# Optimization experiments

Hardware: AMD Instinct MI355X
Metric: run time of the kernel (lower is better)

The kernel has to match this reference:

```python
import jax, jax.numpy as jnp
import numpy as np

HID = 256
BN_EPS = 1e-5
LN_EPS = 1e-5


def setup_inputs() -> dict:
    key = jax.random.key(0)
    ks = jax.random.split(key, 32)
    N, E, B = 50000, 400000, 2048
    F_ATOM, F_PROT = 70, 480

    def lin(k, fi, fo):
        return jax.random.normal(k, (fi, fo), jnp.float32) / np.sqrt(fi).astype(np.float32)

    inp = {
        "x": jax.random.normal(ks[0], (N, F_ATOM), jnp.float32),
        "edge_index": jax.random.randint(ks[1], (2, E), 0, N, jnp.int64),
        "batch": jnp.sort(jax.random.randint(ks[2], (N,), 0, B, jnp.int64)),
        "protein_emb": jax.random.normal(ks[3], (B, F_PROT), jnp.float32),
        # GIN layer 0 (70 -> 256)
        "gin0_w1": lin(ks[4], F_ATOM, HID), "gin0_b1": jnp.zeros((HID,), jnp.float32),
        "gin0_w2": lin(ks[5], HID, HID),    "gin0_b2": jnp.zeros((HID,), jnp.float32),
        "gin0_gamma": jnp.ones((HID,), jnp.float32), "gin0_beta": jnp.zeros((HID,), jnp.float32),
        # GIN layers 1..3 stacked (256 -> 256)
        "gin_w1": jnp.stack([lin(ks[6 + i], HID, HID) for i in range(3)]),
        "gin_b1": jnp.zeros((3, HID), jnp.float32),
        "gin_w2": jnp.stack([lin(ks[9 + i], HID, HID) for i in range(3)]),
        "gin_b2": jnp.zeros((3, HID), jnp.float32),
        "gin_gamma": jnp.ones((3, HID), jnp.float32),
        "gin_beta": jnp.zeros((3, HID), jnp.float32),
        # protein projector
        "wp": lin(ks[12], F_PROT, HID), "bp": jnp.zeros((HID,), jnp.float32),
        "ln_g": jnp.ones((HID,), jnp.float32), "ln_b": jnp.zeros((HID,), jnp.float32),
        # predictor MLP
        "wpr1": lin(ks[13], 2 * HID, 1024), "bpr1": jnp.zeros((1024,), jnp.float32),
        "wpr2": lin(ks[14], 1024, 512),     "bpr2": jnp.zeros((512,), jnp.float32),
        "wpr3": lin(ks[15], 512, 1),        "bpr3": jnp.zeros((1,), jnp.float32),
    }
    return inp


def _gin_layer(h, src, dst, n_nodes, w1, b1, w2, b2, gamma, beta):
    # GINConv (eps=0): mlp(x + sum_{j->i} x_j); scatter-add over destination
    agg = jax.ops.segment_sum(h[src], dst, num_segments=n_nodes)
    z = h + agg
    z = jax.nn.relu(z @ w1 + b1) @ w2 + b2
    # BatchNorm1d in eval mode: running_mean=0, running_var=1
    z = z * (gamma / np.sqrt(1.0 + BN_EPS).astype(np.float32)) + beta
    return jax.nn.relu(z)  # dropout is identity in eval


def reference(x, edge_index, batch, protein_emb,
              gin0_w1, gin0_b1, gin0_w2, gin0_b2, gin0_gamma, gin0_beta,
              gin_w1, gin_b1, gin_w2, gin_b2, gin_gamma, gin_beta,
              wp, bp, ln_g, ln_b,
              wpr1, bpr1, wpr2, bpr2, wpr3, bpr3):
    n_nodes = x.shape[0]
    n_graphs = protein_emb.shape[0]
    src, dst = edge_index[0], edge_index[1]

    h = _gin_layer(x, src, dst, n_nodes, gin0_w1, gin0_b1, gin0_w2, gin0_b2, gin0_gamma, gin0_beta)
    for i in range(3):  # layers 1..3 with residual
        h = h + _gin_layer(h, src, dst, n_nodes,
                           gin_w1[i], gin_b1[i], gin_w2[i], gin_b2[i], gin_gamma[i], gin_beta[i])

    # global_add_pool over graph ids
    drug_vec = jax.ops.segment_sum(h, batch, num_segments=n_graphs)  # [B, 256]

    # protein projector: Linear -> LayerNorm -> ReLU (dropout identity)
    p = protein_emb @ wp + bp
    mu = jnp.mean(p, axis=-1, keepdims=True)
    var = jnp.var(p, axis=-1, keepdims=True)
    p = (p - mu) * jax.lax.rsqrt(var + LN_EPS) * ln_g + ln_b
    prot_vec = jax.nn.relu(p)

    cat = jnp.concatenate([drug_vec, prot_vec], axis=1)  # [B, 512]
    h1 = jax.nn.relu(cat @ wpr1 + bpr1)
    h2 = jax.nn.relu(h1 @ wpr2 + bpr2)
    return h2 @ wpr3 + bpr3  # [B, 1]
```

## Files before the change

kernel.cpp:

```cpp
#include <hip/hip_runtime.h>

#define F_ATOM 70

#define FLAG_RELU 1
#define FLAG_BN   2
#define FLAG_RES  4

typedef __attribute__((ext_vector_type(8))) short short8;
typedef __attribute__((ext_vector_type(4))) float floatx4;

__device__ __forceinline__ float bf2f(unsigned short u) {
    union { unsigned int i; float f; } x; x.i = (unsigned int)u << 16; return x.f;
}
__device__ __forceinline__ unsigned short f2bf(float f) {
    union { float f; unsigned int i; } x; x.f = f;
    unsigned int r = x.i + 0x7fffu + ((x.i >> 16) & 1u);
    return (unsigned short)(r >> 16);
}
__device__ __forceinline__ float blo(unsigned int u){ union{unsigned int a; float f;}x; x.a=u<<16; return x.f; }
__device__ __forceinline__ float bhi(unsigned int u){ union{unsigned int a; float f;}x; x.a=u&0xffff0000u; return x.f; }


__global__ void count_kernel(const int* __restrict__ dst, int* __restrict__ cnt, int E) {
    int i = blockIdx.x * blockDim.x + threadIdx.x;
    if (i < E) atomicAdd(&cnt[dst[i]], 1);
}

__global__ void scan_kernel(const int* __restrict__ cnt, int* __restrict__ offs, int n) {
    __shared__ int wsum[16];
    __shared__ int carry_s;
    int t = threadIdx.x, lane = t & 63, wid = t >> 6;
    if (t == 0) carry_s = 0;
    __syncthreads();
    for (int base = 0; base < n; base += 1024) {
        int idx = base + t;
        int v = (idx < n) ? cnt[idx] : 0;
        int s = v;
        #pragma unroll
        for (int o = 1; o < 64; o <<= 1) {
            int x = __shfl_up(s, o);
            if (lane >= o) s += x;
        }
        if (lane == 63) wsum[wid] = s;
        __syncthreads();
        int woff = 0;
        #pragma unroll
        for (int wI = 0; wI < 16; ++wI) woff += (wI < wid) ? wsum[wI] : 0;
        int carry = carry_s;
        if (idx < n) offs[idx] = carry + woff + s - v;
        __syncthreads();
        if (t == 1023) carry_s = carry + woff + s;
        __syncthreads();
    }
    if (threadIdx.x == 0) offs[n] = carry_s;
}

__global__ void fill_kernel(const int* __restrict__ src, const int* __restrict__ dst,
                            const int* __restrict__ offs, int* __restrict__ cursor,
                            int* __restrict__ ssrc, int E) {
    int i = blockIdx.x * blockDim.x + threadIdx.x;
    if (i < E) {
        int d = dst[i];
        int pos = atomicAdd(&cursor[d], 1);
        ssrc[offs[d] + pos] = src[i];
    }
}

__global__ void graph_bounds_kernel(const int* __restrict__ batch, int* __restrict__ goffs,
                                    int N, int B) {
    int g = blockIdx.x * blockDim.x + threadIdx.x;
    if (g > B) return;
    int lo = 0, hi = N;
    while (lo < hi) {
        int mid = (lo + hi) >> 1;
        if (batch[mid] < g) lo = mid + 1; else hi = mid;
    }
    goffs[g] = lo;
}


__global__ void wtrans_kernel(const float* __restrict__ src, unsigned short* __restrict__ dst,
                              int K, int NC, int Kpad, int L) {
    int idx = blockIdx.x * blockDim.x + threadIdx.x;
    int per = NC * Kpad;
    if (idx >= per * L) return;
    int l = idx / per; int r2 = idx - l * per;
    int nrow = r2 / Kpad, k = r2 - nrow * Kpad;
    float v = (k < K) ? src[(size_t)l * K * NC + (size_t)k * NC + nrow] : 0.f;
    dst[idx] = f2bf(v);
}

__global__ void cvt_kernel(const float* __restrict__ src, unsigned short* __restrict__ dst, int n) {
    int i = blockIdx.x * blockDim.x + threadIdx.x;
    if (i < n) dst[i] = f2bf(src[i]);
}

__global__ void agg0_kernel(const float* __restrict__ x, const int* __restrict__ offs,
                            const int* __restrict__ ssrc, unsigned short* __restrict__ z0, int n) {
    long long idx = (long long)blockIdx.x * blockDim.x + threadIdx.x;
    if (idx >= (long long)n * 128) return;
    int node = (int)(idx >> 7);
    int f = (int)(idx & 127);
    float a = 0.f;
    if (f < F_ATOM) {
        a = x[(long long)node * F_ATOM + f];
        int s = offs[node], e = offs[node + 1];
        for (int i = s; i < e; ++i) a += x[(long long)ssrc[i] * F_ATOM + f];
    }
    z0[idx] = f2bf(a);
}

__global__ void agg_bf16_kernel(const unsigned short* __restrict__ h, const int* __restrict__ offs,
                                const int* __restrict__ ssrc, unsigned short* __restrict__ out, int n) {
    int t = threadIdx.x;
    int node = blockIdx.x * 8 + (t >> 5);
    if (node >= n) return;
    int f8 = (t & 31) * 8;
    uint4 v = *(const uint4*)(h + (size_t)node * 256 + f8);
    float acc[8];
    acc[0]=blo(v.x); acc[1]=bhi(v.x); acc[2]=blo(v.y); acc[3]=bhi(v.y);
    acc[4]=blo(v.z); acc[5]=bhi(v.z); acc[6]=blo(v.w); acc[7]=bhi(v.w);
    int s = offs[node], e = offs[node + 1];
    for (int i = s; i < e; ++i) {
        uint4 u = *(const uint4*)(h + (size_t)ssrc[i] * 256 + f8);
        acc[0]+=blo(u.x); acc[1]+=bhi(u.x); acc[2]+=blo(u.y); acc[3]+=bhi(u.y);
        acc[4]+=blo(u.z); acc[5]+=bhi(u.z); acc[6]+=blo(u.w); acc[7]+=bhi(u.w);
    }
    unsigned int o0 = (unsigned int)f2bf(acc[0]) | ((unsigned int)f2bf(acc[1]) << 16);
    unsigned int o1 = (unsigned int)f2bf(acc[2]) | ((unsigned int)f2bf(acc[3]) << 16);
    unsigned int o2 = (unsigned int)f2bf(acc[4]) | ((unsigned int)f2bf(acc[5]) << 16);
    unsigned int o3 = (unsigned int)f2bf(acc[6]) | ((unsigned int)f2bf(acc[7]) << 16);
    *(uint4*)(out + (size_t)node * 256 + f8) = make_uint4(o0, o1, o2, o3);
}


template<int KSH>
__global__ __launch_bounds__(512) void fused_gin(
    const unsigned short* __restrict__ Z, const unsigned short* __restrict__ W1,
    const float* __restrict__ b1, const unsigned short* __restrict__ W2,
    const float* __restrict__ b2, const float* __restrict__ bng,
    const float* __restrict__ bnb, const unsigned short* __restrict__ res,
    unsigned short* __restrict__ out, int M)
{
    constexpr int CPR = KSH / 8;
    constexpr int NT1 = KSH / 32;
    __shared__ unsigned short sZ[128 * 256];
    const int T = threadIdx.x;
    const int lane = T & 63;
    const int w = T >> 6, wr = w >> 2, wc = w & 3;
    const int fr = lane & 15, hi = lane >> 4;
    const int crow = hi * 4;
    const int row0 = blockIdx.x * 128;

    #pragma unroll
    for (int i = 0; i < (128 * CPR) / 512; ++i) {
        int c = T + i * 512;
        int row = c / CPR, p = c % CPR;
        int pp = p ^ (row & 15);
        int gr = row0 + row; if (gr > M - 1) gr = M - 1;
        __builtin_amdgcn_global_load_lds(
            (const __attribute__((address_space(1))) void*)(Z + (size_t)gr * KSH + pp * 8),
            (__attribute__((address_space(3))) void*)&sZ[c * 8], 16, 0, 0);
    }
    __syncthreads();

    floatx4 acc[4][4];
    #pragma unroll
    for (int m = 0; m < 4; ++m)
        #pragma unroll
        for (int n = 0; n < 4; ++n)
            acc[m][n] = (floatx4){0.f, 0.f, 0.f, 0.f};

    {
        short8 cur[4], nxt[4];
        #pragma unroll
        for (int n = 0; n < 4; ++n)
            cur[n] = *(const short8*)(W1 + (size_t)(wc * 64 + n * 16 + fr) * KSH + hi * 8);
        #pragma unroll
        for (int kk = 0; kk < NT1; ++kk) {
            if (kk + 1 < NT1) {
                #pragma unroll
                for (int n = 0; n < 4; ++n)
                    nxt[n] = *(const short8*)(W1 + (size_t)(wc * 64 + n * 16 + fr) * KSH + (kk + 1) * 32 + hi * 8);
            }
            short8 af[4];
            #pragma unroll
            for (int m = 0; m < 4; ++m) {
                int r = wr * 64 + m * 16 + fr;
                int byte = r * (KSH * 2) + ((kk * 64 + hi * 16) ^ ((r & 15) << 4));
                af[m] = *(const short8*)((const char*)sZ + byte);
            }
            #pragma unroll
            for (int m = 0; m < 4; ++m)
                #pragma unroll
                for (int n = 0; n < 4; ++n)
                    acc[m][n] = __builtin_amdgcn_mfma_f32_16x16x32_bf16(af[m], cur[n], acc[m][n], 0, 0, 0);
            #pragma unroll
            for (int n = 0; n < 4; ++n) cur[n] = nxt[n];
        }
    }
    __syncthreads();

    #pragma unroll
    for (int n = 0; n < 4; ++n) {
        int col = wc * 64 + n * 16 + fr;
        float bb = b1[col];
        #pragma unroll
        for (int m = 0; m < 4; ++m) {
            #pragma unroll
            for (int j = 0; j < 4; ++j) {
                int r = wr * 64 + m * 16 + crow + j;
                float y = fmaxf(acc[m][n][j] + bb, 0.f);
                int byte = r * 512 + ((col * 2) ^ ((r & 15) << 4));
                *(unsigned short*)((char*)sZ + byte) = f2bf(y);
            }
        }
    }
    __syncthreads();

    #pragma unroll
    for (int m = 0; m < 4; ++m)
        #pragma unroll
        for (int n = 0; n < 4; ++n)
            acc[m][n] = (floatx4){0.f, 0.f, 0.f, 0.f};
    {
        short8 cur[4], nxt[4];
        #pragma unroll
        for (int n = 0; n < 4; ++n)
            cur[n] = *(const short8*)(W2 + (size_t)(wc * 64 + n * 16 + fr) * 256 + hi * 8);
        #pragma unroll
        for (int kk = 0; kk < 8; ++kk) {
            if (kk < 7) {
                #pragma unroll
                for (int n = 0; n < 4; ++n)
                    nxt[n] = *(const short8*)(W2 + (size_t)(wc * 64 + n * 16 + fr) * 256 + (kk + 1) * 32 + hi * 8);
            }
            short8 af[4];
            #pragma unroll
            for (int m = 0; m < 4; ++m) {
                int r = wr * 64 + m * 16 + fr;
                int byte = r * 512 + ((kk * 64 + hi * 16) ^ ((r & 15) << 4));
                af[m] = *(const short8*)((const char*)sZ + byte);
            }
            #pragma unroll
            for (int m = 0; m < 4; ++m)
                #pragma unroll
                for (int n = 0; n < 4; ++n)
                    acc[m][n] = __builtin_amdgcn_mfma_f32_16x16x32_bf16(af[m], cur[n], acc[m][n], 0, 0, 0);
            #pragma unroll
            for (int n = 0; n < 4; ++n) cur[n] = nxt[n];
        }
    }
    __syncthreads();

    {
        const float inv = rsqrtf(1.f + 1e-5f);
        #pragma unroll
        for (int n = 0; n < 4; ++n) {
            int col = wc * 64 + n * 16 + fr;
            float bb = b2[col];
            float sc = bng[col] * inv, be = bnb[col];
            #pragma unroll
            for (int m = 0; m < 4; ++m) {
                #pragma unroll
                for (int j = 0; j < 4; ++j) {
                    int r = wr * 64 + m * 16 + crow + j;
                    float y = (acc[m][n][j] + bb) * sc + be;
                    y = fmaxf(y, 0.f);
                    int byte = r * 512 + ((col * 2) ^ ((r & 15) << 4));
                    *(unsigned short*)((char*)sZ + byte) = f2bf(y);
                }
            }
        }
    }
    __syncthreads();

    #pragma unroll
    for (int i = 0; i < 8; ++i) {
        int c = T + i * 512;
        int row = c >> 5, slot = c & 31;
        int gr = row0 + row;
        if (gr >= M) continue;
        int byte = row * 512 + ((slot * 16) ^ ((row & 15) << 4));
        short8 v = *(const short8*)((const char*)sZ + byte);
        if (res) {
            short8 rv = *(const short8*)(res + (size_t)gr * 256 + slot * 8);
            #pragma unroll
            for (int e = 0; e < 8; ++e) {
                float f = bf2f((unsigned short)v[e]) + bf2f((unsigned short)rv[e]);
                v[e] = (short)f2bf(f);
            }
        }
        *(short8*)(out + (size_t)gr * 256 + slot * 8) = v;
    }
}


__global__ __launch_bounds__(256) void mfma_gemm(
    const unsigned short* __restrict__ A, const unsigned short* __restrict__ Bt,
    const float* __restrict__ bias, const float* __restrict__ bng,
    const float* __restrict__ bnb, const unsigned short* __restrict__ res,
    unsigned short* __restrict__ out, int M, int K, int NC, int flags)
{
    __shared__ unsigned short sA[2][128 * 32];
    __shared__ unsigned short sB[2][128 * 32];
    const int T = threadIdx.x;
    const int lane = T & 63;
    const int w = T >> 6, wr = w >> 1, wc = w & 1;
    const int row0 = blockIdx.x * 128;
    const int col0 = blockIdx.y * 128;
    const int nt = K >> 5;

    floatx4 acc[4][4];
    #pragma unroll
    for (int m = 0; m < 4; ++m)
        #pragma unroll
        for (int n = 0; n < 4; ++n)
            acc[m][n] = (floatx4){0.f, 0.f, 0.f, 0.f};

    auto stage = [&](int buf, int k0) {
        #pragma unroll
        for (int it = 0; it < 2; ++it) {
            int c = T + it * 256;
            int r = c >> 2, p = c & 3;
            int gr = row0 + r; if (gr > M - 1) gr = M - 1;
            const unsigned short* gA = A + (size_t)gr * K + k0 + p * 8;
            __builtin_amdgcn_global_load_lds(
                (const __attribute__((address_space(1))) void*)gA,
                (__attribute__((address_space(3))) void*)&sA[buf][c * 8], 16, 0, 0);
            const unsigned short* gB = Bt + (size_t)(col0 + r) * K + k0 + p * 8;
            __builtin_amdgcn_global_load_lds(
                (const __attribute__((address_space(1))) void*)gB,
                (__attribute__((address_space(3))) void*)&sB[buf][c * 8], 16, 0, 0);
        }
    };

    auto compute = [&](int buf) {
        const int fr = lane & 15;
        const int kh = (lane >> 4) * 8;
        short8 af[4], bv[4];
        #pragma unroll
        for (int m = 0; m < 4; ++m)
            af[m] = *(const short8*)&sA[buf][(wr * 64 + m * 16 + fr) * 32 + kh];
        #pragma unroll
        for (int n = 0; n < 4; ++n)
            bv[n] = *(const short8*)&sB[buf][(wc * 64 + n * 16 + fr) * 32 + kh];
        #pragma unroll
        for (int m = 0; m < 4; ++m)
            #pragma unroll
            for (int n = 0; n < 4; ++n)
                acc[m][n] = __builtin_amdgcn_mfma_f32_16x16x32_bf16(af[m], bv[n], acc[m][n], 0, 0, 0);
    };

    stage(0, 0);
    __syncthreads();
    int cur = 0;
    for (int t = 0; t < nt - 1; ++t) {
        stage(cur ^ 1, (t + 1) * 32);
        compute(cur);
        __syncthreads();
        cur ^= 1;
    }
    compute(cur);

    const int crow = (lane >> 4) * 4;
    const int ccol = lane & 15;
    const float inv = rsqrtf(1.f + 1e-5f);
    #pragma unroll
    for (int n = 0; n < 4; ++n) {
        int col = col0 + wc * 64 + n * 16 + ccol;
        float bb = bias ? bias[col] : 0.f;
        float sc = 1.f, be = 0.f;
        if (flags & FLAG_BN) { sc = bng[col] * inv; be = bnb[col]; }
        #pragma unroll
        for (int m = 0; m < 4; ++m) {
            #pragma unroll
            for (int j = 0; j < 4; ++j) {
                int r = row0 + wr * 64 + m * 16 + crow + j;
                if (r >= M) continue;
                float y = acc[m][n][j] + bb;
                if (flags & FLAG_BN) y = y * sc + be;
                if (flags & FLAG_RELU) y = fmaxf(y, 0.f);
                if (flags & FLAG_RES) y += bf2f(res[(size_t)r * NC + col]);
                out[(size_t)r * NC + col] = f2bf(y);
            }
        }
    }
}


__global__ void pool_kernel(const unsigned short* __restrict__ h, const int* __restrict__ goffs,
                            unsigned short* __restrict__ out, int ldout) {
    int g = blockIdx.x;
    int f = threadIdx.x;
    int s = goffs[g], e = goffs[g + 1];
    float acc = 0.f;
    for (int i = s; i < e; ++i) acc += bf2f(h[(size_t)i * 256 + f]);
    out[(size_t)g * ldout + f] = f2bf(acc);
}

__global__ void ln_relu_kernel(const unsigned short* __restrict__ p, const float* __restrict__ g,
                               const float* __restrict__ b, unsigned short* __restrict__ out, int ldout) {
    int row = blockIdx.x;
    int t = threadIdx.x;
    float v = bf2f(p[(size_t)row * 256 + t]);
    float s1 = v, s2 = v * v;
    #pragma unroll
    for (int o = 32; o > 0; o >>= 1) { s1 += __shfl_xor(s1, o); s2 += __shfl_xor(s2, o); }
    __shared__ float as1[4], as2[4];
    int w = t >> 6, lane = t & 63;
    if (lane == 0) { as1[w] = s1; as2[w] = s2; }
    __syncthreads();
    float tot1 = as1[0] + as1[1] + as1[2] + as1[3];
    float tot2 = as2[0] + as2[1] + as2[2] + as2[3];
    float mean = tot1 * (1.f / 256.f);
    float var = tot2 * (1.f / 256.f) - mean * mean;
    float y = (v - mean) * rsqrtf(var + 1e-5f) * g[t] + b[t];
    out[(size_t)row * ldout + t] = f2bf(fmaxf(y, 0.f));
}

__global__ void pred3_kernel(const unsigned short* __restrict__ h2, const float* __restrict__ w,
                             const float* __restrict__ b, float* __restrict__ out, int B) {
    int row = blockIdx.x * 4 + (threadIdx.x >> 6);
    int lane = threadIdx.x & 63;
    if (row >= B) return;
    float acc = 0.f;
    #pragma unroll
    for (int k = 0; k < 512; k += 64) acc += bf2f(h2[(size_t)row * 512 + k + lane]) * w[k + lane];
    #pragma unroll
    for (int o = 32; o > 0; o >>= 1) acc += __shfl_xor(acc, o);
    if (lane == 0) out[row] = acc + b[0];
}


extern "C" void kernel_launch(void* const* d_in, const int* in_sizes, int n_in,
                              void* d_out, int out_size, void* d_ws, size_t ws_size,
                              hipStream_t stream) {
    const float* x    = (const float*)d_in[0];
    const int*   ei   = (const int*)d_in[1];
    const int*   batch= (const int*)d_in[2];
    const float* pemb = (const float*)d_in[3];
    const float* g0w1 = (const float*)d_in[4];
    const float* g0b1 = (const float*)d_in[5];
    const float* g0w2 = (const float*)d_in[6];
    const float* g0b2 = (const float*)d_in[7];
    const float* g0g  = (const float*)d_in[8];
    const float* g0be = (const float*)d_in[9];
    const float* gw1  = (const float*)d_in[10];
    const float* gb1  = (const float*)d_in[11];
    const float* gw2  = (const float*)d_in[12];
    const float* gb2  = (const float*)d_in[13];
    const float* gg   = (const float*)d_in[14];
    const float* gbe  = (const float*)d_in[15];
    const float* wp   = (const float*)d_in[16];
    const float* bp   = (const float*)d_in[17];
    const float* lng  = (const float*)d_in[18];
    const float* lnb  = (const float*)d_in[19];
    const float* wpr1 = (const float*)d_in[20];
    const float* bpr1 = (const float*)d_in[21];
    const float* wpr2 = (const float*)d_in[22];
    const float* bpr2 = (const float*)d_in[23];
    const float* wpr3 = (const float*)d_in[24];
    const float* bpr3 = (const float*)d_in[25];

    int N = in_sizes[0] / F_ATOM;
    int E = in_sizes[1] / 2;
    int B = in_sizes[3] / 480;

    char* wsp = (char*)d_ws;
    auto carve = [&](size_t bytes) {
        void* p = (void*)wsp;
        wsp += (bytes + 255) & ~(size_t)255;
        return p;
    };
    int* offs   = (int*)carve((size_t)(N + 1) * 4);
    int* cursor = (int*)carve((size_t)N * 4);
    int* ssrc   = (int*)carve((size_t)E * 4);
    int* goffs  = (int*)carve((size_t)(B + 1) * 4);
    unsigned short* z0   = (unsigned short*)carve((size_t)N * 128 * 2);
    unsigned short* hbuf = (unsigned short*)carve((size_t)N * 256 * 2);
    unsigned short* tbuf = (unsigned short*)carve((size_t)N * 256 * 2);
    unsigned short* zbuf = (unsigned short*)carve((size_t)N * 256 * 2);
    unsigned short* pembbf = (unsigned short*)carve((size_t)B * 480 * 2);
    unsigned short* ptmp = (unsigned short*)carve((size_t)B * 256 * 2);
    unsigned short* cat  = (unsigned short*)carve((size_t)B * 512 * 2);
    unsigned short* h1   = (unsigned short*)carve((size_t)B * 1024 * 2);
    unsigned short* h2   = (unsigned short*)carve((size_t)B * 512 * 2);
    unsigned short* w10t = (unsigned short*)carve((size_t)256 * 128 * 2);
    unsigned short* w20t = (unsigned short*)carve((size_t)256 * 256 * 2);
    unsigned short* w1t  = (unsigned short*)carve((size_t)3 * 256 * 256 * 2);
    unsigned short* w2t  = (unsigned short*)carve((size_t)3 * 256 * 256 * 2);
    unsigned short* wpt  = (unsigned short*)carve((size_t)256 * 480 * 2);
    unsigned short* wpr1t= (unsigned short*)carve((size_t)1024 * 512 * 2);
    unsigned short* wpr2t= (unsigned short*)carve((size_t)512 * 1024 * 2);

    const int* srcp = ei;
    const int* dstp = ei + E;

    hipMemsetAsync(cursor, 0, (size_t)N * 4, stream);
    count_kernel<<<(E + 255) / 256, 256, 0, stream>>>(dstp, cursor, E);
    scan_kernel<<<1, 1024, 0, stream>>>(cursor, offs, N);
    hipMemsetAsync(cursor, 0, (size_t)N * 4, stream);
    fill_kernel<<<(E + 255) / 256, 256, 0, stream>>>(srcp, dstp, offs, cursor, ssrc, E);
    graph_bounds_kernel<<<(B + 256) / 256, 256, 0, stream>>>(batch, goffs, N, B);

    auto WT = [&](const float* s, unsigned short* d, int K, int NC, int Kpad, int L) {
        wtrans_kernel<<<(NC * Kpad * L + 255) / 256, 256, 0, stream>>>(s, d, K, NC, Kpad, L);
    };
    WT(g0w1, w10t, 70, 256, 128, 1);
    WT(g0w2, w20t, 256, 256, 256, 1);
    WT(gw1, w1t, 256, 256, 256, 3);
    WT(gw2, w2t, 256, 256, 256, 3);
    WT(wp, wpt, 480, 256, 480, 1);
    WT(wpr1, wpr1t, 512, 1024, 512, 1);
    WT(wpr2, wpr2t, 1024, 512, 1024, 1);
    cvt_kernel<<<(B * 480 + 255) / 256, 256, 0, stream>>>(pemb, pembbf, B * 480);

    int rbN = (N + 127) / 128;

    agg0_kernel<<<(int)(((long long)N * 128 + 255) / 256), 256, 0, stream>>>(x, offs, ssrc, z0, N);
    fused_gin<128><<<rbN, 512, 0, stream>>>(z0, w10t, g0b1, w20t, g0b2, g0g, g0be,
                                            nullptr, hbuf, N);

    unsigned short* H = hbuf; unsigned short* T2 = tbuf;
    for (int i = 0; i < 3; ++i) {
        agg_bf16_kernel<<<(N + 7) / 8, 256, 0, stream>>>(H, offs, ssrc, zbuf, N);
        fused_gin<256><<<rbN, 512, 0, stream>>>(zbuf, w1t + (size_t)i * 65536, gb1 + i * 256,
                                                w2t + (size_t)i * 65536, gb2 + i * 256,
                                                gg + i * 256, gbe + i * 256, H, T2, N);
        unsigned short* tmp = H; H = T2; T2 = tmp;
    }

    pool_kernel<<<B, 256, 0, stream>>>(H, goffs, cat, 512);

    mfma_gemm<<<dim3((B + 127) / 128, 2), 256, 0, stream>>>(pembbf, wpt, bp, nullptr, nullptr, nullptr,
                                                            ptmp, B, 480, 256, 0);
    ln_relu_kernel<<<B, 256, 0, stream>>>(ptmp, lng, lnb, cat + 256, 512);

    mfma_gemm<<<dim3((B + 127) / 128, 8), 256, 0, stream>>>(cat, wpr1t, bpr1, nullptr, nullptr, nullptr,
                                                            h1, B, 512, 1024, FLAG_RELU);
    mfma_gemm<<<dim3((B + 127) / 128, 4), 256, 0, stream>>>(h1, wpr2t, bpr2, nullptr, nullptr, nullptr,
                                                            h2, B, 1024, 512, FLAG_RELU);
    pred3_kernel<<<(B + 3) / 4, 256, 0, stream>>>(h2, wpr3, bpr3, (float*)d_out, B);
}
```

Measured before the change: 606.3 us.

## Fuse neighbor aggregation into GIN MLP kernel prologue via LDS staging

Removes the separate aggregation kernels. Each fused GIN block now gathers neighbor rows through the CSR, sums them in fp32 and writes the bf16 result straight into swizzled shared memory before the MFMA stages. Layer 0 first converts x to bf16 padded to 80 columns instead of gathering fp32 rows. This avoids writing and re-reading the intermediate aggregate buffer and saves launches, but the gather now runs inside a kernel with high LDS use and few blocks (N/128), which may limit latency hiding for the irregular loads. Layer-0 aggregation now accumulates bf16-rounded inputs rather than fp32 x.

```diff
diff --git a/kernel.cpp b/kernel.cpp
--- a/kernel.cpp
+++ b/kernel.cpp
@@ -95,55 +95,30 @@
     if (i < n) dst[i] = f2bf(src[i]);
 }
 
-__global__ void agg0_kernel(const float* __restrict__ x, const int* __restrict__ offs,
-                            const int* __restrict__ ssrc, unsigned short* __restrict__ z0, int n) {
+__global__ void cvt_pad_kernel(const float* __restrict__ x, unsigned short* __restrict__ xb, int N) {
     long long idx = (long long)blockIdx.x * blockDim.x + threadIdx.x;
-    if (idx >= (long long)n * 128) return;
-    int node = (int)(idx >> 7);
-    int f = (int)(idx & 127);
-    float a = 0.f;
-    if (f < F_ATOM) {
-        a = x[(long long)node * F_ATOM + f];
-        int s = offs[node], e = offs[node + 1];
-        for (int i = s; i < e; ++i) a += x[(long long)ssrc[i] * F_ATOM + f];
-    }
-    z0[idx] = f2bf(a);
-}
-
-__global__ void agg_bf16_kernel(const unsigned short* __restrict__ h, const int* __restrict__ offs,
-                                const int* __restrict__ ssrc, unsigned short* __restrict__ out, int n) {
-    int t = threadIdx.x;
-    int node = blockIdx.x * 8 + (t >> 5);
-    if (node >= n) return;
-    int f8 = (t & 31) * 8;
-    uint4 v = *(const uint4*)(h + (size_t)node * 256 + f8);
-    float acc[8];
-    acc[0]=blo(v.x); acc[1]=bhi(v.x); acc[2]=blo(v.y); acc[3]=bhi(v.y);
-    acc[4]=blo(v.z); acc[5]=bhi(v.z); acc[6]=blo(v.w); acc[7]=bhi(v.w);
-    int s = offs[node], e = offs[node + 1];
-    for (int i = s; i < e; ++i) {
-        uint4 u = *(const uint4*)(h + (size_t)ssrc[i] * 256 + f8);
-        acc[0]+=blo(u.x); acc[1]+=bhi(u.x); acc[2]+=blo(u.y); acc[3]+=bhi(u.y);
-        acc[4]+=blo(u.z); acc[5]+=bhi(u.z); acc[6]+=blo(u.w); acc[7]+=bhi(u.w);
-    }
-    unsigned int o0 = (unsigned int)f2bf(acc[0]) | ((unsigned int)f2bf(acc[1]) << 16);
-    unsigned int o1 = (unsigned int)f2bf(acc[2]) | ((unsigned int)f2bf(acc[3]) << 16);
-    unsigned int o2 = (unsigned int)f2bf(acc[4]) | ((unsigned int)f2bf(acc[5]) << 16);
-    unsigned int o3 = (unsigned int)f2bf(acc[6]) | ((unsigned int)f2bf(acc[7]) << 16);
-    *(uint4*)(out + (size_t)node * 256 + f8) = make_uint4(o0, o1, o2, o3);
-}
-
-
-template<int KSH>
+    if (idx >= (long long)N * 80) return;
+    int node = (int)(idx / 80);
+    int f = (int)(idx - (long long)node * 80);
+    float v = (f < F_ATOM) ? x[(long long)node * F_ATOM + f] : 0.f;
+    xb[idx] = f2bf(v);
+}
+
+
+template<int KSH, int SRCW>
 __global__ __launch_bounds__(512) void fused_gin(
-    const unsigned short* __restrict__ Z, const unsigned short* __restrict__ W1,
-    const float* __restrict__ b1, const unsigned short* __restrict__ W2,
-    const float* __restrict__ b2, const float* __restrict__ bng,
-    const float* __restrict__ bnb, const unsigned short* __restrict__ res,
+    const unsigned short* __restrict__ SRC,
+    const int* __restrict__ offs, const int* __restrict__ ssrc,
+    const unsigned short* __restrict__ W1, const float* __restrict__ b1,
+    const unsigned short* __restrict__ W2, const float* __restrict__ b2,
+    const float* __restrict__ bng, const float* __restrict__ bnb,
+    const unsigned short* __restrict__ res,
     unsigned short* __restrict__ out, int M)
 {
     constexpr int CPR = KSH / 8;
     constexpr int NT1 = KSH / 32;
+    constexpr int NSLOT = (128 * CPR) / 512;
+    constexpr int LIVE = SRCW / 8;
     __shared__ unsigned short sZ[128 * 256];
     const int T = threadIdx.x;
     const int lane = T & 63;
@@ -153,14 +128,41 @@
     const int row0 = blockIdx.x * 128;
 
     #pragma unroll
-    for (int i = 0; i < (128 * CPR) / 512; ++i) {
-        int c = T + i * 512;
-        int row = c / CPR, p = c % CPR;
-        int pp = p ^ (row & 15);
-        int gr = row0 + row; if (gr > M - 1) gr = M - 1;
-        __builtin_amdgcn_global_load_lds(
-            (const __attribute__((address_space(1))) void*)(Z + (size_t)gr * KSH + pp * 8),
-            (__attribute__((address_space(3))) void*)&sZ[c * 8], 16, 0, 0);
+    for (int i = 0; i < NSLOT; ++i) {
+        int slot = T + i * 512;
+        int row = slot / CPR, chunk = slot % CPR;
+        int node = row0 + row; if (node > M - 1) node = M - 1;
+        float a[8];
+        #pragma unroll
+        for (int e = 0; e < 8; ++e) a[e] = 0.f;
+        if (LIVE == CPR || chunk < LIVE) {
+            uint4 v = *(const uint4*)(SRC + (size_t)node * SRCW + chunk * 8);
+            a[0]=blo(v.x); a[1]=bhi(v.x); a[2]=blo(v.y); a[3]=bhi(v.y);
+            a[4]=blo(v.z); a[5]=bhi(v.z); a[6]=blo(v.w); a[7]=bhi(v.w);
+            int s = offs[node], e2 = offs[node + 1];
+            int k = s;
+            for (; k + 1 < e2; k += 2) {
+                int n0 = ssrc[k], n1 = ssrc[k + 1];
+                uint4 u0 = *(const uint4*)(SRC + (size_t)n0 * SRCW + chunk * 8);
+                uint4 u1 = *(const uint4*)(SRC + (size_t)n1 * SRCW + chunk * 8);
+                a[0]+=blo(u0.x); a[1]+=bhi(u0.x); a[2]+=blo(u0.y); a[3]+=bhi(u0.y);
+                a[4]+=blo(u0.z); a[5]+=bhi(u0.z); a[6]+=blo(u0.w); a[7]+=bhi(u0.w);
+                a[0]+=blo(u1.x); a[1]+=bhi(u1.x); a[2]+=blo(u1.y); a[3]+=bhi(u1.y);
+                a[4]+=blo(u1.z); a[5]+=bhi(u1.z); a[6]+=blo(u1.w); a[7]+=bhi(u1.w);
+            }
+            if (k < e2) {
+                int n0 = ssrc[k];
+                uint4 u0 = *(const uint4*)(SRC + (size_t)n0 * SRCW + chunk * 8);
+                a[0]+=blo(u0.x); a[1]+=bhi(u0.x); a[2]+=blo(u0.y); a[3]+=bhi(u0.y);
+                a[4]+=blo(u0.z); a[5]+=bhi(u0.z); a[6]+=blo(u0.w); a[7]+=bhi(u0.w);
+            }
+        }
+        unsigned int o0 = (unsigned int)f2bf(a[0]) | ((unsigned int)f2bf(a[1]) << 16);
+        unsigned int o1 = (unsigned int)f2bf(a[2]) | ((unsigned int)f2bf(a[3]) << 16);
+        unsigned int o2 = (unsigned int)f2bf(a[4]) | ((unsigned int)f2bf(a[5]) << 16);
+        unsigned int o3 = (unsigned int)f2bf(a[6]) | ((unsigned int)f2bf(a[7]) << 16);
+        int byte = row * (KSH * 2) + ((chunk * 16) ^ ((row & 15) << 4));
+        *(uint4*)((char*)sZ + byte) = make_uint4(o0, o1, o2, o3);
     }
     __syncthreads();
 
@@ -477,10 +479,9 @@
     int* cursor = (int*)carve((size_t)N * 4);
     int* ssrc   = (int*)carve((size_t)E * 4);
     int* goffs  = (int*)carve((size_t)(B + 1) * 4);
-    unsigned short* z0   = (unsigned short*)carve((size_t)N * 128 * 2);
+    unsigned short* xb   = (unsigned short*)carve((size_t)N * 80 * 2);
     unsigned short* hbuf = (unsigned short*)carve((size_t)N * 256 * 2);
     unsigned short* tbuf = (unsigned short*)carve((size_t)N * 256 * 2);
-    unsigned short* zbuf = (unsigned short*)carve((size_t)N * 256 * 2);
     unsigned short* pembbf = (unsigned short*)carve((size_t)B * 480 * 2);
     unsigned short* ptmp = (unsigned short*)carve((size_t)B * 256 * 2);
     unsigned short* cat  = (unsigned short*)carve((size_t)B * 512 * 2);
@@ -515,19 +516,19 @@
     WT(wpr1, wpr1t, 512, 1024, 512, 1);
     WT(wpr2, wpr2t, 1024, 512, 1024, 1);
     cvt_kernel<<<(B * 480 + 255) / 256, 256, 0, stream>>>(pemb, pembbf, B * 480);
+    cvt_pad_kernel<<<(int)(((long long)N * 80 + 255) / 256), 256, 0, stream>>>(x, xb, N);
 
     int rbN = (N + 127) / 128;
 
-    agg0_kernel<<<(int)(((long long)N * 128 + 255) / 256), 256, 0, stream>>>(x, offs, ssrc, z0, N);
-    fused_gin<128><<<rbN, 512, 0, stream>>>(z0, w10t, g0b1, w20t, g0b2, g0g, g0be,
-                                            nullptr, hbuf, N);
+    fused_gin<128, 80><<<rbN, 512, 0, stream>>>(xb, offs, ssrc, w10t, g0b1, w20t, g0b2,
+                                                g0g, g0be, nullptr, hbuf, N);
 
     unsigned short* H = hbuf; unsigned short* T2 = tbuf;
     for (int i = 0; i < 3; ++i) {
-        agg_bf16_kernel<<<(N + 7) / 8, 256, 0, stream>>>(H, offs, ssrc, zbuf, N);
-        fused_gin<256><<<rbN, 512, 0, stream>>>(zbuf, w1t + (size_t)i * 65536, gb1 + i * 256,
-                                                w2t + (size_t)i * 65536, gb2 + i * 256,
-                                                gg + i * 256, gbe + i * 256, H, T2, N);
+        fused_gin<256, 256><<<rbN, 512, 0, stream>>>(H, offs, ssrc,
+                                                     w1t + (size_t)i * 65536, gb1 + i * 256,
+                                                     w2t + (size_t)i * 65536, gb2 + i * 256,
+                                                     gg + i * 256, gbe + i * 256, H, T2, N);
         unsigned short* tmp = H; H = T2; T2 = tmp;
     }
 
```

After: 654.0 us. 7.9% more time.

## Convert atom features to padded bf16 and vectorize layer-0 aggregation; unroll gathers

Applied to the files above, without the earlier changes.

Adds a pass that converts the fp32 atom features into a bf16 buffer padded to 80 columns. Layer-0 aggregation then uses 16-byte vector gathers with 16 threads per node instead of one scalar fp32 load per thread per feature. Both aggregation kernels now unroll the neighbor loop by four so several gathers are in flight at once. The fused GIN kernel gets a min-blocks hint in its launch bounds, and neighbor sums in layer 0 are now built from bf16-rounded inputs, which slightly changes precision.

```diff
diff --git a/kernel.cpp b/kernel.cpp
--- a/kernel.cpp
+++ b/kernel.cpp
@@ -95,47 +95,101 @@
     if (i < n) dst[i] = f2bf(src[i]);
 }
 
-__global__ void agg0_kernel(const float* __restrict__ x, const int* __restrict__ offs,
-                            const int* __restrict__ ssrc, unsigned short* __restrict__ z0, int n) {
+__global__ void cvt_pad_kernel(const float* __restrict__ x, unsigned short* __restrict__ xb, int N) {
     long long idx = (long long)blockIdx.x * blockDim.x + threadIdx.x;
-    if (idx >= (long long)n * 128) return;
-    int node = (int)(idx >> 7);
-    int f = (int)(idx & 127);
-    float a = 0.f;
-    if (f < F_ATOM) {
-        a = x[(long long)node * F_ATOM + f];
-        int s = offs[node], e = offs[node + 1];
-        for (int i = s; i < e; ++i) a += x[(long long)ssrc[i] * F_ATOM + f];
-    }
-    z0[idx] = f2bf(a);
-}
-
-__global__ void agg_bf16_kernel(const unsigned short* __restrict__ h, const int* __restrict__ offs,
-                                const int* __restrict__ ssrc, unsigned short* __restrict__ out, int n) {
+    if (idx >= (long long)N * 80) return;
+    int node = (int)(idx / 80);
+    int f = (int)(idx - (long long)node * 80);
+    float v = (f < F_ATOM) ? x[(long long)node * F_ATOM + f] : 0.f;
+    xb[idx] = f2bf(v);
+}
+
+__global__ __launch_bounds__(256) void agg0b_kernel(
+    const unsigned short* __restrict__ xb, const int* __restrict__ offs,
+    const int* __restrict__ ssrc, unsigned short* __restrict__ z0, int n) {
+    int t = threadIdx.x;
+    int node = blockIdx.x * 16 + (t >> 4);
+    if (node >= n) return;
+    int c = t & 15;
+    if (c >= 10) {
+        *(uint4*)(z0 + (size_t)node * 128 + c * 8) = make_uint4(0, 0, 0, 0);
+        return;
+    }
+    const unsigned short* base = xb + (size_t)node * 80 + c * 8;
+    uint4 v = *(const uint4*)base;
+    float a[8];
+    a[0]=blo(v.x); a[1]=bhi(v.x); a[2]=blo(v.y); a[3]=bhi(v.y);
+    a[4]=blo(v.z); a[5]=bhi(v.z); a[6]=blo(v.w); a[7]=bhi(v.w);
+    int s = offs[node], e2 = offs[node + 1];
+    int k = s;
+    for (; k + 3 < e2; k += 4) {
+        uint4 u0 = *(const uint4*)(xb + (size_t)ssrc[k]     * 80 + c * 8);
+        uint4 u1 = *(const uint4*)(xb + (size_t)ssrc[k + 1] * 80 + c * 8);
+        uint4 u2 = *(const uint4*)(xb + (size_t)ssrc[k + 2] * 80 + c * 8);
+        uint4 u3 = *(const uint4*)(xb + (size_t)ssrc[k + 3] * 80 + c * 8);
+        a[0]+=blo(u0.x); a[1]+=bhi(u0.x); a[2]+=blo(u0.y); a[3]+=bhi(u0.y);
+        a[4]+=blo(u0.z); a[5]+=bhi(u0.z); a[6]+=blo(u0.w); a[7]+=bhi(u0.w);
+        a[0]+=blo(u1.x); a[1]+=bhi(u1.x); a[2]+=blo(u1.y); a[3]+=bhi(u1.y);
+        a[4]+=blo(u1.z); a[5]+=bhi(u1.z); a[6]+=blo(u1.w); a[7]+=bhi(u1.w);
+        a[0]+=blo(u2.x); a[1]+=bhi(u2.x); a[2]+=blo(u2.y); a[3]+=bhi(u2.y);
+        a[4]+=blo(u2.z); a[5]+=bhi(u2.z); a[6]+=blo(u2.w); a[7]+=bhi(u2.w);
+        a[0]+=blo(u3.x); a[1]+=bhi(u3.x); a[2]+=blo(u3.y); a[3]+=bhi(u3.y);
+        a[4]+=blo(u3.z); a[5]+=bhi(u3.z); a[6]+=blo(u3.w); a[7]+=bhi(u3.w);
+    }
+    for (; k < e2; ++k) {
+        uint4 u0 = *(const uint4*)(xb + (size_t)ssrc[k] * 80 + c * 8);
+        a[0]+=blo(u0.x); a[1]+=bhi(u0.x); a[2]+=blo(u0.y); a[3]+=bhi(u0.y);
+        a[4]+=blo(u0.z); a[5]+=bhi(u0.z); a[6]+=blo(u0.w); a[7]+=bhi(u0.w);
+    }
+    unsigned int o0 = (unsigned int)f2bf(a[0]) | ((unsigned int)f2bf(a[1]) << 16);
+    unsigned int o1 = (unsigned int)f2bf(a[2]) | ((unsigned int)f2bf(a[3]) << 16);
+    unsigned int o2 = (unsigned int)f2bf(a[4]) | ((unsigned int)f2bf(a[5]) << 16);
+    unsigned int o3 = (unsigned int)f2bf(a[6]) | ((unsigned int)f2bf(a[7]) << 16);
+    *(uint4*)(z0 + (size_t)node * 128 + c * 8) = make_uint4(o0, o1, o2, o3);
+}
+
+__global__ __launch_bounds__(256) void agg_bf16_kernel(
+    const unsigned short* __restrict__ h, const int* __restrict__ offs,
+    const int* __restrict__ ssrc, unsigned short* __restrict__ out, int n) {
     int t = threadIdx.x;
     int node = blockIdx.x * 8 + (t >> 5);
     if (node >= n) return;
     int f8 = (t & 31) * 8;
     uint4 v = *(const uint4*)(h + (size_t)node * 256 + f8);
-    float acc[8];
-    acc[0]=blo(v.x); acc[1]=bhi(v.x); acc[2]=blo(v.y); acc[3]=bhi(v.y);
-    acc[4]=blo(v.z); acc[5]=bhi(v.z); acc[6]=blo(v.w); acc[7]=bhi(v.w);
-    int s = offs[node], e = offs[node + 1];
-    for (int i = s; i < e; ++i) {
-        uint4 u = *(const uint4*)(h + (size_t)ssrc[i] * 256 + f8);
-        acc[0]+=blo(u.x); acc[1]+=bhi(u.x); acc[2]+=blo(u.y); acc[3]+=bhi(u.y);
-        acc[4]+=blo(u.z); acc[5]+=bhi(u.z); acc[6]+=blo(u.w); acc[7]+=bhi(u.w);
-    }
-    unsigned int o0 = (unsigned int)f2bf(acc[0]) | ((unsigned int)f2bf(acc[1]) << 16);
-    unsigned int o1 = (unsigned int)f2bf(acc[2]) | ((unsigned int)f2bf(acc[3]) << 16);
-    unsigned int o2 = (unsigned int)f2bf(acc[4]) | ((unsigned int)f2bf(acc[5]) << 16);
-    unsigned int o3 = (unsigned int)f2bf(acc[6]) | ((unsigned int)f2bf(acc[7]) << 16);
+    float a[8];
+    a[0]=blo(v.x); a[1]=bhi(v.x); a[2]=blo(v.y); a[3]=bhi(v.y);
+    a[4]=blo(v.z); a[5]=bhi(v.z); a[6]=blo(v.w); a[7]=bhi(v.w);
+    int s = offs[node], e2 = offs[node + 1];
+    int k = s;
+    for (; k + 3 < e2; k += 4) {
+        uint4 u0 = *(const uint4*)(h + (size_t)ssrc[k]     * 256 + f8);
+        uint4 u1 = *(const uint4*)(h + (size_t)ssrc[k + 1] * 256 + f8);
+        uint4 u2 = *(const uint4*)(h + (size_t)ssrc[k + 2] * 256 + f8);
+        uint4 u3 = *(const uint4*)(h + (size_t)ssrc[k + 3] * 256 + f8);
+        a[0]+=blo(u0.x); a[1]+=bhi(u0.x); a[2]+=blo(u0.y); a[3]+=bhi(u0.y);
+        a[4]+=blo(u0.z); a[5]+=bhi(u0.z); a[6]+=blo(u0.w); a[7]+=bhi(u0.w);
+        a[0]+=blo(u1.x); a[1]+=bhi(u1.x); a[2]+=blo(u1.y); a[3]+=bhi(u1.y);
+        a[4]+=blo(u1.z); a[5]+=bhi(u1.z); a[6]+=blo(u1.w); a[7]+=bhi(u1.w);
+        a[0]+=blo(u2.x); a[1]+=bhi(u2.x); a[2]+=blo(u2.y); a[3]+=bhi(u2.y);
+        a[4]+=blo(u2.z); a[5]+=bhi(u2.z); a[6]+=blo(u2.w); a[7]+=bhi(u2.w);
+        a[0]+=blo(u3.x); a[1]+=bhi(u3.x); a[2]+=blo(u3.y); a[3]+=bhi(u3.y);
+        a[4]+=blo(u3.z); a[5]+=bhi(u3.z); a[6]+=blo(u3.w); a[7]+=bhi(u3.w);
+    }
+    for (; k < e2; ++k) {
+        uint4 u0 = *(const uint4*)(h + (size_t)ssrc[k] * 256 + f8);
+        a[0]+=blo(u0.x); a[1]+=bhi(u0.x); a[2]+=blo(u0.y); a[3]+=bhi(u0.y);
+        a[4]+=blo(u0.z); a[5]+=bhi(u0.z); a[6]+=blo(u0.w); a[7]+=bhi(u0.w);
+    }
+    unsigned int o0 = (unsigned int)f2bf(a[0]) | ((unsigned int)f2bf(a[1]) << 16);
+    unsigned int o1 = (unsigned int)f2bf(a[2]) | ((unsigned int)f2bf(a[3]) << 16);
+    unsigned int o2 = (unsigned int)f2bf(a[4]) | ((unsigned int)f2bf(a[5]) << 16);
+    unsigned int o3 = (unsigned int)f2bf(a[6]) | ((unsigned int)f2bf(a[7]) << 16);
     *(uint4*)(out + (size_t)node * 256 + f8) = make_uint4(o0, o1, o2, o3);
 }
 
 
 template<int KSH>
-__global__ __launch_bounds__(512) void fused_gin(
+__global__ __launch_bounds__(512, 4) void fused_gin(
     const unsigned short* __restrict__ Z, const unsigned short* __restrict__ W1,
     const float* __restrict__ b1, const unsigned short* __restrict__ W2,
     const float* __restrict__ b2, const float* __restrict__ bng,
@@ -477,6 +531,7 @@
     int* cursor = (int*)carve((size_t)N * 4);
     int* ssrc   = (int*)carve((size_t)E * 4);
     int* goffs  = (int*)carve((size_t)(B + 1) * 4);
+    unsigned short* xb   = (unsigned short*)carve((size_t)N * 80 * 2);
     unsigned short* z0   = (unsigned short*)carve((size_t)N * 128 * 2);
     unsigned short* hbuf = (unsigned short*)carve((size_t)N * 256 * 2);
     unsigned short* tbuf = (unsigned short*)carve((size_t)N * 256 * 2);
@@ -515,10 +570,11 @@
     WT(wpr1, wpr1t, 512, 1024, 512, 1);
     WT(wpr2, wpr2t, 1024, 512, 1024, 1);
     cvt_kernel<<<(B * 480 + 255) / 256, 256, 0, stream>>>(pemb, pembbf, B * 480);
+    cvt_pad_kernel<<<(int)(((long long)N * 80 + 255) / 256), 256, 0, stream>>>(x, xb, N);
 
     int rbN = (N + 127) / 128;
 
-    agg0_kernel<<<(int)(((long long)N * 128 + 255) / 256), 256, 0, stream>>>(x, offs, ssrc, z0, N);
+    agg0b_kernel<<<(N + 15) / 16, 256, 0, stream>>>(xb, offs, ssrc, z0, N);
     fused_gin<128><<<rbN, 512, 0, stream>>>(z0, w10t, g0b1, w20t, g0b2, g0g, g0be,
                                             nullptr, hbuf, N);
 
```

Result: faster. 573.2 us (-5.5%).
